# Optimization experiments

Hardware: AMD Instinct MI355X
Metric: run time of the kernel (lower is better)

The kernel has to match this reference:

```python
import jax, jax.numpy as jnp
import numpy as np

B, L, E, H = 2, 2048, 1024, 16
D = E // H  # head dim = 64


def setup_inputs() -> dict:
    key = jax.random.key(0)
    ks = jax.random.split(key, 10)
    s = 0.02
    return {
        "xt": jax.random.normal(ks[0], (B, L, E), jnp.float32),
        "xs": jax.random.normal(ks[1], (B, L, E), jnp.float32),
        "Wt": jax.random.normal(ks[2], (E, 3 * E), jnp.float32) * s,  # t_attn weight (x @ Wt)
        "bt": jnp.zeros((3 * E,), jnp.float32),
        "Ws": jax.random.normal(ks[3], (E, 2 * E), jnp.float32) * s,  # s_attn weight
        "bs": jnp.zeros((2 * E,), jnp.float32),
        "Wc": jax.random.normal(ks[4], (E, E), jnp.float32) * s,      # c_proj weight
        "bc": jnp.zeros((E,), jnp.float32),
        "lam_ts": jnp.ones((1,), jnp.float32),
        "lam_st": jnp.ones((1,), jnp.float32),
        "lam_ss": jnp.ones((1,), jnp.float32),
    }


def _heads(x):
    # (B, L, E) -> (B, H, L, D)
    return x.reshape(B, L, H, D).transpose(0, 2, 1, 3)


def reference(xt, xs, Wt, bt, Ws, bs, Wc, bc, lam_ts, lam_st, lam_ss):
    qt, kt, vt = jnp.split(xt @ Wt + bt, 3, axis=2)
    qs, ks = jnp.split(xs @ Ws + bs, 2, axis=2)
    qt, kt, vt, qs, ks = map(_heads, (qt, kt, vt, qs, ks))

    # 4-way disentangled scores; fuse the 4 matmuls into 2 by combining keys:
    # qt@kt^T + lam_ts*qt@ks^T = qt @ (kt + lam_ts*ks)^T
    # lam_st*qs@kt^T + lam_ss*qs@ks^T = qs @ (lam_st*kt + lam_ss*ks)^T
    k1 = kt + lam_ts[0] * ks
    k2 = lam_st[0] * kt + lam_ss[0] * ks
    att = (jnp.einsum('bhqd,bhkd->bhqk', qt, k1)
           + jnp.einsum('bhqd,bhkd->bhqk', qs, k2)) * (1.0 / np.sqrt(D))
    att = jax.nn.softmax(att, axis=-1)
    y = jnp.einsum('bhqk,bhkd->bhqd', att, vt)  # (B, H, L, D)
    y = y.transpose(0, 2, 1, 3).reshape(B, L, E)
    return y @ Wc + bc
```

## Files before the change

### kernel.cpp

```cpp
#include <hip/hip_runtime.h>
#include <math.h>

#define LQ 2048
#define EQ 1024
#define M_ROWS 4096
#define BH 32

typedef _Float16 f16x8 __attribute__((ext_vector_type(8)));
typedef _Float16 f16x4 __attribute__((ext_vector_type(4)));
typedef _Float16 f16x2 __attribute__((ext_vector_type(2)));
typedef float f32x4 __attribute__((ext_vector_type(4)));
typedef float f32x16 __attribute__((ext_vector_type(16)));

#define QSCALE 0.1803368801111204f
#define DEFER_THR 8.0f

__device__ __forceinline__ void async_ld16(const _Float16* g, _Float16* l) {
  __builtin_amdgcn_global_load_lds(
      (const __attribute__((address_space(1))) unsigned int*)g,
      (__attribute__((address_space(3))) unsigned int*)l, 16, 0, 0);
}

__global__ __launch_bounds__(256) void prep(
    const float* __restrict__ xt, const float* __restrict__ xs,
    const float* __restrict__ Wt, const float* __restrict__ Ws,
    const float* __restrict__ Wc,
    _Float16* __restrict__ xt16, _Float16* __restrict__ xs16,
    _Float16* __restrict__ WtT, _Float16* __restrict__ WsT,
    _Float16* __restrict__ WcT) {
  int gb = blockIdx.x;
  if (gb < 4096) {
    int i = gb * 256 + threadIdx.x;
    const float* s; _Float16* d; size_t off;
    if (i < 524288) { s = xt; d = xt16; off = (size_t)i * 8; }
    else            { s = xs; d = xs16; off = (size_t)(i - 524288) * 8; }
    float4 a = *(const float4*)&s[off];
    float4 b = *(const float4*)&s[off + 4];
    f16x8 h;
    h[0] = (_Float16)a.x; h[1] = (_Float16)a.y; h[2] = (_Float16)a.z; h[3] = (_Float16)a.w;
    h[4] = (_Float16)b.x; h[5] = (_Float16)b.y; h[6] = (_Float16)b.z; h[7] = (_Float16)b.w;
    *(f16x8*)&d[off] = h;
  } else {
    __shared__ float T[32][65];
    int tb = gb - 4096;
    int c0 = (tb % 96) * 64;
    int k0 = (tb / 96) * 32;
    const float* W; _Float16* D; int Nw, cl;
    if (c0 < 3072)      { W = Wt; D = WtT; Nw = 3072; cl = c0; }
    else if (c0 < 5120) { W = Ws; D = WsT; Nw = 2048; cl = c0 - 3072; }
    else                { W = Wc; D = WcT; Nw = 1024; cl = c0 - 5120; }
    const int tid = threadIdx.x;
#pragma unroll
    for (int p = 0; p < 4; ++p) {
      int idx = tid + p * 256;
      int row = idx >> 5;
      int c2 = (idx & 31) * 2;
      float2 v = *(const float2*)&W[(size_t)(k0 + row) * Nw + cl + c2];
      T[row][c2] = v.x;
      T[row][c2 + 1] = v.y;
    }
    __syncthreads();
#pragma unroll
    for (int p = 0; p < 4; ++p) {
      int idx = tid + p * 256;
      int col = idx >> 4;
      int k2 = (idx & 15) * 2;
      f16x2 h2;
      h2[0] = (_Float16)T[k2][col];
      h2[1] = (_Float16)T[k2 + 1][col];
      *(f16x2*)&D[(size_t)(cl + col) * 1024 + k0 + k2] = h2;
    }
  }
}

__global__ __launch_bounds__(256, 3) void proj_gemm(
    const _Float16* __restrict__ xt16, const _Float16* __restrict__ xs16,
    const _Float16* __restrict__ WtT, const _Float16* __restrict__ WsT,
    const float* __restrict__ bt, const float* __restrict__ bs,
    _Float16* __restrict__ q16, _Float16* __restrict__ k16,
    _Float16* __restrict__ v16) {
  __shared__ _Float16 LS[128 * 128];
  _Float16* Al0 = LS;
  _Float16* Bl0 = LS + 4096;
  _Float16* Al1 = LS + 8192;
  _Float16* Bl1 = LS + 12288;

  const int tid = threadIdx.x;
  const int w = tid >> 6;
  const int lane = tid & 63;
  const int quad = lane >> 4;
  const int l15 = lane & 15;
  const int wm = w >> 1, wn = w & 1;

  const int wg = blockIdx.y * 16 + blockIdx.x;
  const int swz = (wg & 7) * 160 + (wg >> 3);
  const int bx = swz & 15;
  const int by = swz >> 4;
  const int n0 = bx * 128;

  const _Float16* Ab;
  const _Float16* Bb;
  const float* bias;
  int m0, bsel = 0, branch;
  if (by < 32) {
    branch = 0; Ab = xt16; Bb = WtT; bias = bt; m0 = by * 128;
  } else if (by < 48) {
    branch = 1;
    int by2 = by - 32;
    bsel = by2 >> 3;
    m0 = (by2 & 7) * 128;
    Ab = WtT + (size_t)2048 * 1024;
    Bb = xt16 + (size_t)bsel * 2048 * 1024;
    bias = bt;
  } else {
    branch = 2; Ab = xs16; Bb = WsT; bias = bs; m0 = (by - 48) * 128;
  }

  const int srow = lane >> 2;
  const int schunk = ((lane & 3) ^ ((lane >> 3) & 3)) * 8;
  const int key = (l15 >> 1) & 3;

  f32x4 acc[4][4];
#pragma unroll
  for (int mb = 0; mb < 4; ++mb)
#pragma unroll
    for (int nb = 0; nb < 4; ++nb) acc[mb][nb] = (f32x4){0.f, 0.f, 0.f, 0.f};

  auto dma = [&](int kt, _Float16* Al, _Float16* Bl) {
#pragma unroll
    for (int i = 0; i < 2; ++i) {
      int rt = w * 32 + i * 16;
      async_ld16(&Ab[(size_t)(m0 + rt + srow) * 1024 + kt + schunk], &Al[rt * 32]);
      async_ld16(&Bb[(size_t)(n0 + rt + srow) * 1024 + kt + schunk], &Bl[rt * 32]);
    }
  };

  auto comp = [&](const _Float16* Al, const _Float16* Bl) {
    f16x8 af[4], bf[4];
    const int pc = (quad ^ key) * 8;
#pragma unroll
    for (int mb = 0; mb < 4; ++mb)
      af[mb] = *(const f16x8*)&Al[(wm * 64 + mb * 16 + l15) * 32 + pc];
#pragma unroll
    for (int nb = 0; nb < 4; ++nb)
      bf[nb] = *(const f16x8*)&Bl[(wn * 64 + nb * 16 + l15) * 32 + pc];
#pragma unroll
    for (int mb = 0; mb < 4; ++mb)
#pragma unroll
      for (int nb = 0; nb < 4; ++nb)
        acc[mb][nb] = __builtin_amdgcn_mfma_f32_16x16x32_f16(bf[nb], af[mb], acc[mb][nb], 0, 0, 0);
  };

  dma(0, Al0, Bl0);
  for (int kt = 0; kt < 1024; kt += 64) {
    __syncthreads();
    dma(kt + 32, Al1, Bl1);
    comp(Al0, Bl0);
    __syncthreads();
    if (kt + 64 < 1024) dma(kt + 64, Al0, Bl0);
    comp(Al1, Bl1);
  }

  __syncthreads();
#pragma unroll
  for (int mb = 0; mb < 4; ++mb) {
    const int rowL = wm * 64 + mb * 16 + l15;
    const int rx = (rowL & 7) << 3;
    float rbias = 0.f;
    if (branch == 1) rbias = bias[2048 + m0 + rowL];
#pragma unroll
    for (int nb = 0; nb < 4; ++nb) {
      const int colL = wn * 64 + nb * 16 + quad * 4;
      f16x4 o4;
      if (branch == 1) {
#pragma unroll
        for (int r = 0; r < 4; ++r) o4[r] = (_Float16)(acc[mb][nb][r] + rbias);
      } else {
        const float4 bv4 = *(const float4*)&bias[n0 + colL];
        o4[0] = (_Float16)(acc[mb][nb][0] + bv4.x);
        o4[1] = (_Float16)(acc[mb][nb][1] + bv4.y);
        o4[2] = (_Float16)(acc[mb][nb][2] + bv4.z);
        o4[3] = (_Float16)(acc[mb][nb][3] + bv4.w);
      }
      *(f16x4*)&LS[rowL * 128 + (colL ^ rx)] = o4;
    }
  }
  __syncthreads();

  const int g = tid & 15;
  const int c8 = g * 8;
#pragma unroll
  for (int p = 0; p < 8; ++p) {
    const int r = p * 16 + (tid >> 4);
    f16x8 v8 = *(const f16x8*)&LS[r * 128 + (c8 ^ ((r & 7) << 3))];
    if (branch == 1) {
      *(f16x8*)&v16[(size_t)(bsel * 1024 + m0 + r) * 2048 + n0 + c8] = v8;
    } else {
      const int grow = m0 + r;
      const int col = n0 + c8;
      const int bb = grow >> 11, ll = grow & 2047;
      const int which = col >> 10, e = col & 1023;
      const int hh = e >> 6, dd = e & 63;
      _Float16* dst = which ? k16 : q16;
      const int off = (branch == 0) ? 0 : 64;
      *(f16x8*)&dst[((size_t)(bb * 16 + hh) * 2048 + ll) * 128 + off + dd] = v8;
    }
  }
}

__global__ __launch_bounds__(256, 3) void cproj_gemm(
    const _Float16* __restrict__ A, const _Float16* __restrict__ Bm,
    const float* __restrict__ bias, float* __restrict__ outf) {
  __shared__ _Float16 Al0[128 * 32];
  __shared__ _Float16 Bl0[64 * 32];
  __shared__ _Float16 Al1[128 * 32];
  __shared__ _Float16 Bl1[64 * 32];

  const int tid = threadIdx.x;
  const int w = tid >> 6;
  const int lane = tid & 63;
  const int quad = lane >> 4;
  const int l15 = lane & 15;
  const int wm = w >> 1, wn = w & 1;
  const int m0 = blockIdx.y * 128;
  const int n0 = blockIdx.x * 64;

  const int srow = lane >> 2;
  const int schunk = ((lane & 3) ^ ((lane >> 3) & 3)) * 8;

  f32x4 acc[4][2];
#pragma unroll
  for (int mb = 0; mb < 4; ++mb)
#pragma unroll
    for (int nb = 0; nb < 2; ++nb) acc[mb][nb] = (f32x4){0.f, 0.f, 0.f, 0.f};

  const int key = (l15 >> 1) & 3;

  auto dma = [&](int kt, _Float16* Al, _Float16* Bl) {
#pragma unroll
    for (int i = 0; i < 2; ++i) {
      int rt = w * 32 + i * 16;
      async_ld16(&A[(size_t)(m0 + rt + srow) * 1024 + kt + schunk], &Al[rt * 32]);
    }
    int rtb = w * 16;
    async_ld16(&Bm[(size_t)(n0 + rtb + srow) * 1024 + kt + schunk], &Bl[rtb * 32]);
  };

  auto comp = [&](const _Float16* Al, const _Float16* Bl) {
    f16x8 af[4], bf[2];
    const int pc = (quad ^ key) * 8;
#pragma unroll
    for (int mb = 0; mb < 4; ++mb)
      af[mb] = *(const f16x8*)&Al[(wm * 64 + mb * 16 + l15) * 32 + pc];
#pragma unroll
    for (int nb = 0; nb < 2; ++nb)
      bf[nb] = *(const f16x8*)&Bl[(wn * 32 + nb * 16 + l15) * 32 + pc];
#pragma unroll
    for (int mb = 0; mb < 4; ++mb)
#pragma unroll
      for (int nb = 0; nb < 2; ++nb)
        acc[mb][nb] = __builtin_amdgcn_mfma_f32_16x16x32_f16(bf[nb], af[mb], acc[mb][nb], 0, 0, 0);
  };

  dma(0, Al0, Bl0);
  for (int kt = 0; kt < 1024; kt += 64) {
    __syncthreads();
    dma(kt + 32, Al1, Bl1);
    comp(Al0, Bl0);
    __syncthreads();
    if (kt + 64 < 1024) dma(kt + 64, Al0, Bl0);
    comp(Al1, Bl1);
  }

#pragma unroll
  for (int nb = 0; nb < 2; ++nb) {
    const int col0 = n0 + wn * 32 + nb * 16 + quad * 4;
    const float4 bv4 = *(const float4*)&bias[col0];
#pragma unroll
    for (int mb = 0; mb < 4; ++mb) {
      int row = m0 + wm * 64 + mb * 16 + l15;
      float4 o4;
      o4.x = acc[mb][nb][0] + bv4.x;
      o4.y = acc[mb][nb][1] + bv4.y;
      o4.z = acc[mb][nb][2] + bv4.z;
      o4.w = acc[mb][nb][3] + bv4.w;
      *(float4*)&outf[(size_t)row * 1024 + col0] = o4;
    }
  }
}

__global__ __launch_bounds__(256, 2) void flash_attn_mfma(
    const _Float16* __restrict__ qcat, const _Float16* __restrict__ kcat,
    const _Float16* __restrict__ vT, _Float16* __restrict__ y,
    const float* __restrict__ lam_ts, const float* __restrict__ lam_st,
    const float* __restrict__ lam_ss) {
  const int bh = blockIdx.y;
  const int qt0 = blockIdx.x * 128;
  const int b = bh >> 4, h = bh & 15;
  const _Float16* Qg = qcat + (size_t)bh * LQ * 128;
  const _Float16* Kg = kcat + (size_t)bh * LQ * 128;
  const _Float16* Vg = vT + (size_t)bh * 64 * LQ;

  __shared__ _Float16 Ksh0[64 * 128];
  __shared__ _Float16 Ksh1[64 * 128];
  __shared__ _Float16 Vsh0[64 * 64];
  __shared__ _Float16 Vsh1[64 * 64];
  __shared__ _Float16 Vsh2[64 * 64];
  __shared__ _Float16 Vsh3[64 * 64];

  const int tid = threadIdx.x;
  const int w = tid >> 6;
  const int lane = tid & 63;
  const int half = lane >> 5;
  const int l31 = lane & 31;

  const float lts = lam_ts[0], lst = lam_st[0], lss = lam_ss[0];

  f16x8 qf[8];
#pragma unroll
  for (int db = 0; db < 4; ++db) {
    const _Float16* qp = &Qg[(size_t)(qt0 + w * 32 + l31) * 128 + db * 16 + half * 8];
    f16x8 a = *(const f16x8*)qp;
    f16x8 bq = *(const f16x8*)(qp + 64);
#pragma unroll
    for (int e = 0; e < 8; ++e) {
      float fa = (float)a[e], fb = (float)bq[e];
      qf[db][e]     = (_Float16)(QSCALE * (fa + lst * fb));
      qf[db + 4][e] = (_Float16)(QSCALE * (lts * fa + lss * fb));
    }
  }

  float m_i = -INFINITY;
  float l_i = 0.f;
  f32x16 O[2];
#pragma unroll
  for (int nt = 0; nt < 2; ++nt)
#pragma unroll
    for (int r = 0; r < 16; ++r) O[nt][r] = 0.f;

  auto dma_k = [&](int t, _Float16* Kd) {
#pragma unroll
    for (int a = 0; a < 4; ++a) {
      int row = w * 16 + a * 4 + (lane >> 4);
      int sc = (lane & 15) ^ (row & 7);
      async_ld16(&Kg[(size_t)(t + row) * 128 + sc * 8], &Kd[(w * 16 + a * 4) * 128]);
    }
  };
  auto dma_v = [&](int t, _Float16* Vd) {
#pragma unroll
    for (int a = 0; a < 2; ++a) {
      int row = w * 16 + a * 8 + (lane >> 3);
      int sc = (lane & 7) ^ (row & 7);
      async_ld16(&Vg[(size_t)row * LQ + t + sc * 8], &Vd[(w * 16 + a * 8) * 64]);
    }
  };

  auto qk = [&](const _Float16* Ks, f32x16* Sp) {
    __builtin_amdgcn_s_setprio(1);
#pragma unroll
    for (int db = 0; db < 8; ++db) {
      const int pc = ((db * 2 + half) ^ (lane & 7)) * 8;
      f16x8 af0 = *(const f16x8*)&Ks[(l31) * 128 + pc];
      f16x8 af1 = *(const f16x8*)&Ks[(32 + l31) * 128 + pc];
      Sp[0] = __builtin_amdgcn_mfma_f32_32x32x16_f16(af0, qf[db], Sp[0], 0, 0, 0);
      Sp[1] = __builtin_amdgcn_mfma_f32_32x32x16_f16(af1, qf[db], Sp[1], 0, 0, 0);
    }
    __builtin_amdgcn_s_setprio(0);
  };

  auto softpv = [&](f32x16* S, const _Float16* Vs0, const _Float16* Vs1) {
    float mx = -INFINITY;
#pragma unroll
    for (int kb = 0; kb < 4; ++kb)
#pragma unroll
      for (int r = 0; r < 16; ++r) mx = fmaxf(mx, S[kb][r]);
    mx = fmaxf(mx, __shfl_xor(mx, 32));

    if (__any(mx > m_i + DEFER_THR)) {
      float m_new = fmaxf(m_i, mx);
      float alpha = __builtin_amdgcn_exp2f(m_i - m_new);
      l_i *= alpha;
#pragma unroll
      for (int nt = 0; nt < 2; ++nt)
#pragma unroll
        for (int r = 0; r < 16; ++r) O[nt][r] *= alpha;
      m_i = m_new;
    }

    float s = 0.f;
#pragma unroll
    for (int kb = 0; kb < 4; ++kb)
#pragma unroll
      for (int r = 0; r < 16; ++r) {
        float p = __builtin_amdgcn_exp2f(S[kb][r] - m_i);
        S[kb][r] = p;
        s += p;
      }
    s += __shfl_xor(s, 32);
    l_i += s;

#pragma unroll
    for (int kb = 0; kb < 4; ++kb) {
      unsigned pu[8];
#pragma unroll
      for (int i = 0; i < 8; ++i) {
        f16x2 t2;
        t2[0] = (_Float16)S[kb][2 * i];
        t2[1] = (_Float16)S[kb][2 * i + 1];
        pu[i] = __builtin_bit_cast(unsigned, t2);
      }
#pragma unroll
      for (int c = 0; c < 2; ++c) {
        unsigned u0 = pu[4 * c + 0], u1 = pu[4 * c + 1];
        unsigned u2 = pu[4 * c + 2], u3 = pu[4 * c + 3];
        asm("v_permlane32_swap_b32 %0, %1" : "+v"(u0), "+v"(u2));
        asm("v_permlane32_swap_b32 %0, %1" : "+v"(u1), "+v"(u3));
        union { unsigned u[4]; f16x8 v; } pb;
        pb.u[0] = u0; pb.u[1] = u1; pb.u[2] = u2; pb.u[3] = u3;
        const int kb2 = kb * 2 + c;
        const _Float16* Vs = (kb2 < 4) ? Vs0 : Vs1;
        const int kb2r = kb2 & 3;
        f16x8 av[2];
#pragma unroll
        for (int nt = 0; nt < 2; ++nt) {
          int dim = nt * 32 + l31;
          int pc = ((kb2r * 2 + half) ^ (dim & 7)) * 8;
          av[nt] = *(const f16x8*)&Vs[dim * 64 + pc];
        }
        __builtin_amdgcn_s_setprio(1);
#pragma unroll
        for (int nt = 0; nt < 2; ++nt)
          O[nt] = __builtin_amdgcn_mfma_f32_32x32x16_f16(av[nt], pb.v, O[nt], 0, 0, 0);
        __builtin_amdgcn_s_setprio(0);
      }
    }
  };

  auto step = [&](int t, const _Float16* Vr0, _Float16* Vr1, _Float16* Vw2) {
    f32x16 S[4];
#pragma unroll
    for (int kb = 0; kb < 4; ++kb)
#pragma unroll
      for (int r = 0; r < 16; ++r) S[kb][r] = 0.f;

    __syncthreads();
    dma_k(t + 64, Ksh1);
    dma_v(t + 64, Vr1);
    qk(Ksh0, &S[0]);
    __syncthreads();
    if (t + 128 < LQ) {
      dma_k(t + 128, Ksh0);
      dma_v(t + 128, Vw2);
    }
    qk(Ksh1, &S[2]);
    softpv(S, Vr0, Vr1);
  };

  dma_k(0, Ksh0);
  dma_v(0, Vsh0);
  for (int t = 0; t < LQ; t += 256) {
    step(t,       Vsh0, Vsh1, Vsh2);
    step(t + 128, Vsh2, Vsh3, Vsh0);
  }

  float inv = 1.f / l_i;
  int qrow = qt0 + w * 32 + l31;
#pragma unroll
  for (int nt = 0; nt < 2; ++nt)
#pragma unroll
    for (int rg = 0; rg < 4; ++rg) {
      f16x4 o4;
#pragma unroll
      for (int i = 0; i < 4; ++i) o4[i] = (_Float16)(O[nt][rg * 4 + i] * inv);
      int dim = nt * 32 + rg * 8 + half * 4;
      *(f16x4*)&y[((size_t)b * LQ + qrow) * EQ + h * 64 + dim] = o4;
    }
}

extern "C" void kernel_launch(void* const* d_in, const int* in_sizes, int n_in,
                              void* d_out, int out_size, void* d_ws, size_t ws_size,
                              hipStream_t stream) {
  const float* xt = (const float*)d_in[0];
  const float* xs = (const float*)d_in[1];
  const float* Wt = (const float*)d_in[2];
  const float* bt = (const float*)d_in[3];
  const float* Ws = (const float*)d_in[4];
  const float* bs = (const float*)d_in[5];
  const float* Wc = (const float*)d_in[6];
  const float* bc = (const float*)d_in[7];
  const float* lam_ts = (const float*)d_in[8];
  const float* lam_st = (const float*)d_in[9];
  const float* lam_ss = (const float*)d_in[10];
  float* out = (float*)d_out;

  _Float16* w16 = (_Float16*)d_ws;
  _Float16* xt16 = w16;
  _Float16* xs16 = xt16 + 4194304;
  _Float16* WtT  = xs16 + 4194304;
  _Float16* WsT  = WtT + 3145728;
  _Float16* WcT  = WsT + 2097152;
  _Float16* qcat = WcT + 1048576;
  _Float16* kcat = qcat + 8388608;
  _Float16* vbufT = kcat + 8388608;
  _Float16* ybuf = vbufT + 4194304;

  prep<<<7168, 256, 0, stream>>>(xt, xs, Wt, Ws, Wc, xt16, xs16, WtT, WsT, WcT);
  proj_gemm<<<dim3(16, 80), 256, 0, stream>>>(
      xt16, xs16, WtT, WsT, bt, bs, qcat, kcat, vbufT);
  flash_attn_mfma<<<dim3(16, 32), 256, 0, stream>>>(
      qcat, kcat, vbufT, ybuf, lam_ts, lam_st, lam_ss);
  cproj_gemm<<<dim3(16, 32), 256, 0, stream>>>(ybuf, WcT, bc, out);
}
```

Baseline: 262.4 us.

## Software-pipeline QK of next tile with softmax-PV of current 64-key tile

Restructures the attention main loop so each stage processes 64 keys: the QK^T MMA for the next tile is issued alongside softmax and PV for the previous tile, using double-buffered score registers and a four-slot V ring. It replaces the earlier 128-key step that ran both QK blocks before softmax. The s_setprio hints are also removed. Smaller per-step tiles mean more barriers and more frequent online-softmax max checks, and the extra live score registers may raise register pressure.

Result: faster. 254.6 us (median of 2 runs) (-3.0%).

```diff
diff --git a/kernel.cpp b/kernel.cpp
--- a/kernel.cpp
+++ b/kernel.cpp
@@ -301,12 +301,12 @@
   const _Float16* Kg = kcat + (size_t)bh * LQ * 128;
   const _Float16* Vg = vT + (size_t)bh * 64 * LQ;
 
-  __shared__ _Float16 Ksh0[64 * 128];
-  __shared__ _Float16 Ksh1[64 * 128];
-  __shared__ _Float16 Vsh0[64 * 64];
-  __shared__ _Float16 Vsh1[64 * 64];
-  __shared__ _Float16 Vsh2[64 * 64];
-  __shared__ _Float16 Vsh3[64 * 64];
+  __shared__ _Float16 K0s[64 * 128];
+  __shared__ _Float16 K1s[64 * 128];
+  __shared__ _Float16 V0s[64 * 64];
+  __shared__ _Float16 V1s[64 * 64];
+  __shared__ _Float16 V2s[64 * 64];
+  __shared__ _Float16 V3s[64 * 64];
 
   const int tid = threadIdx.x;
   const int w = tid >> 6;
@@ -356,22 +356,24 @@
   };
 
   auto qk = [&](const _Float16* Ks, f32x16* Sp) {
-    __builtin_amdgcn_s_setprio(1);
+#pragma unroll
+    for (int kb = 0; kb < 2; ++kb)
+#pragma unroll
+      for (int r = 0; r < 16; ++r) Sp[kb][r] = 0.f;
 #pragma unroll
     for (int db = 0; db < 8; ++db) {
       const int pc = ((db * 2 + half) ^ (lane & 7)) * 8;
-      f16x8 af0 = *(const f16x8*)&Ks[(l31) * 128 + pc];
+      f16x8 af0 = *(const f16x8*)&Ks[l31 * 128 + pc];
       f16x8 af1 = *(const f16x8*)&Ks[(32 + l31) * 128 + pc];
       Sp[0] = __builtin_amdgcn_mfma_f32_32x32x16_f16(af0, qf[db], Sp[0], 0, 0, 0);
       Sp[1] = __builtin_amdgcn_mfma_f32_32x32x16_f16(af1, qf[db], Sp[1], 0, 0, 0);
     }
-    __builtin_amdgcn_s_setprio(0);
-  };
-
-  auto softpv = [&](f32x16* S, const _Float16* Vs0, const _Float16* Vs1) {
+  };
+
+  auto softpv = [&](f32x16* S, const _Float16* Vs) {
     float mx = -INFINITY;
 #pragma unroll
-    for (int kb = 0; kb < 4; ++kb)
+    for (int kb = 0; kb < 2; ++kb)
 #pragma unroll
       for (int r = 0; r < 16; ++r) mx = fmaxf(mx, S[kb][r]);
     mx = fmaxf(mx, __shfl_xor(mx, 32));
@@ -389,7 +391,7 @@
 
     float s = 0.f;
 #pragma unroll
-    for (int kb = 0; kb < 4; ++kb)
+    for (int kb = 0; kb < 2; ++kb)
 #pragma unroll
       for (int r = 0; r < 16; ++r) {
         float p = __builtin_amdgcn_exp2f(S[kb][r] - m_i);
@@ -400,7 +402,7 @@
     l_i += s;
 
 #pragma unroll
-    for (int kb = 0; kb < 4; ++kb) {
+    for (int kb = 0; kb < 2; ++kb) {
       unsigned pu[8];
 #pragma unroll
       for (int i = 0; i < 8; ++i) {
@@ -418,50 +420,54 @@
         union { unsigned u[4]; f16x8 v; } pb;
         pb.u[0] = u0; pb.u[1] = u1; pb.u[2] = u2; pb.u[3] = u3;
         const int kb2 = kb * 2 + c;
-        const _Float16* Vs = (kb2 < 4) ? Vs0 : Vs1;
-        const int kb2r = kb2 & 3;
         f16x8 av[2];
 #pragma unroll
         for (int nt = 0; nt < 2; ++nt) {
           int dim = nt * 32 + l31;
-          int pc = ((kb2r * 2 + half) ^ (dim & 7)) * 8;
+          int pc = ((kb2 * 2 + half) ^ (dim & 7)) * 8;
           av[nt] = *(const f16x8*)&Vs[dim * 64 + pc];
         }
-        __builtin_amdgcn_s_setprio(1);
 #pragma unroll
         for (int nt = 0; nt < 2; ++nt)
           O[nt] = __builtin_amdgcn_mfma_f32_32x32x16_f16(av[nt], pb.v, O[nt], 0, 0, 0);
-        __builtin_amdgcn_s_setprio(0);
       }
     }
   };
 
-  auto step = [&](int t, const _Float16* Vr0, _Float16* Vr1, _Float16* Vw2) {
-    f32x16 S[4];
-#pragma unroll
-    for (int kb = 0; kb < 4; ++kb)
-#pragma unroll
-      for (int r = 0; r < 16; ++r) S[kb][r] = 0.f;
-
-    __syncthreads();
-    dma_k(t + 64, Ksh1);
-    dma_v(t + 64, Vr1);
-    qk(Ksh0, &S[0]);
-    __syncthreads();
-    if (t + 128 < LQ) {
-      dma_k(t + 128, Ksh0);
-      dma_v(t + 128, Vw2);
-    }
-    qk(Ksh1, &S[2]);
-    softpv(S, Vr0, Vr1);
-  };
-
-  dma_k(0, Ksh0);
-  dma_v(0, Vsh0);
-  for (int t = 0; t < LQ; t += 256) {
-    step(t,       Vsh0, Vsh1, Vsh2);
-    step(t + 128, Vsh2, Vsh3, Vsh0);
-  }
+  f32x16 Sa[2], Sb[2];
+
+  dma_k(0, K0s);
+  dma_v(0, V0s);
+  __syncthreads();
+  dma_k(64, K1s);
+  dma_v(64, V1s);
+  qk(K0s, Sb);
+
+  for (int j = 0; j < 7; ++j) {
+    const int t = j * 256 + 64;
+    __syncthreads();
+    dma_k(t + 64, K0s);  dma_v(t + 64, V2s);
+    qk(K1s, Sa);  softpv(Sb, V0s);
+    __syncthreads();
+    dma_k(t + 128, K1s); dma_v(t + 128, V3s);
+    qk(K0s, Sb);  softpv(Sa, V1s);
+    __syncthreads();
+    dma_k(t + 192, K0s); dma_v(t + 192, V0s);
+    qk(K1s, Sa);  softpv(Sb, V2s);
+    __syncthreads();
+    dma_k(t + 256, K1s); dma_v(t + 256, V1s);
+    qk(K0s, Sb);  softpv(Sa, V3s);
+  }
+
+  __syncthreads();
+  dma_k(1920, K0s); dma_v(1920, V2s);
+  qk(K1s, Sa);  softpv(Sb, V0s);
+  __syncthreads();
+  dma_k(1984, K1s); dma_v(1984, V3s);
+  qk(K0s, Sb);  softpv(Sa, V1s);
+  __syncthreads();
+  qk(K1s, Sa);  softpv(Sb, V2s);
+  softpv(Sa, V3s);
 
   float inv = 1.f / l_i;
   int qrow = qt0 + w * 32 + l31;
```
